# Performance work log

Hardware: AMD Instinct MI355X
Metric: run time of the kernel (lower is better)

Reference implementation:

```python
import jax, jax.numpy as jnp
import numpy as np

N, T, U, V = 8, 200, 50, 500
BLANK = 0
EPS = 1e-10


def setup_inputs() -> dict:
    key = jax.random.key(0)
    k1, k2, k3, k4, k5 = jax.random.split(key, 5)
    logits = jax.random.normal(k1, (N, T, U, V), jnp.float32)
    teacher_logits = jax.random.normal(k2, (N, T, U, V), jnp.float32)
    y = jax.random.randint(k3, (N, U), 1, V)            # padded labels (blank=0 used as pad)
    x_lens = jax.random.randint(k4, (N,), T // 2, T + 1)  # valid encoder frames
    y_lens = jax.random.randint(k5, (N,), U // 2, U + 1)  # valid label lengths
    return {"logits": logits, "teacher_logits": teacher_logits, "y": y,
            "x_lens": x_lens, "y_lens": y_lens}


def reference(logits, teacher_logits, y, x_lens, y_lens):
    # Efficient RNNT-KD: collapse V-dim softmax into 3 classes (label, blank, rest).
    n, t, u, v = logits.shape
    s = jax.nn.softmax(logits, axis=-1)             # (N,T,U,V)
    te = jax.nn.softmax(teacher_logits, axis=-1)    # (N,T,U,V)

    idx = jnp.broadcast_to(y[:, None, :, None], (n, t, u, 1))  # label index per (n,t,u)
    py = jnp.take_along_axis(s, idx, axis=-1)       # (N,T,U,1)
    t_py = jnp.take_along_axis(te, idx, axis=-1)
    blank = s[..., BLANK:BLANK + 1]
    t_blank = te[..., BLANK:BLANK + 1]

    rem = 1.0 - py - blank
    t_rem = 1.0 - t_py - t_blank
    t_rem = jnp.where(t_rem < 0, EPS, t_rem)        # floor negative remainders (in-place set in torch)

    student = jnp.log(jnp.clip(jnp.concatenate([py, blank, rem], axis=-1), EPS, 1.0))  # (N,T,U,3)
    teacher = jnp.concatenate([t_py, t_blank, t_rem], axis=-1)                          # (N,T,U,3)

    t_mask = (jnp.arange(t)[None, :] < x_lens[:, None]).astype(student.dtype)[:, :, None, None]
    u_mask = (jnp.arange(u)[None, :] < y_lens[:, None]).astype(student.dtype)[:, None, :, None]
    m = t_mask * u_mask
    return jnp.stack([student * m, teacher * m])    # (2,N,T,U,3)
```

## Files before the change

kernel.cpp:

```cpp
#include <hip/hip_runtime.h>

#define N_ 8
#define T_ 200
#define U_ 50
#define V_ 500
#define NTU (N_ * T_ * U_)
#define EPSF 1e-10f

__global__ __launch_bounds__(256) void tkd_kernel(
    const float* __restrict__ lg,
    const float* __restrict__ tl,
    const int* __restrict__ y,
    const int* __restrict__ xlen,
    const int* __restrict__ ylen,
    float* __restrict__ out)
{
    const int tid = threadIdx.x;
    const int l   = tid & 15;
    const int row = blockIdx.x * 16 + (tid >> 4);

    const int n  = row / (T_ * U_);
    const int r2 = row - n * (T_ * U_);
    const int t  = r2 / U_;
    const int u  = r2 - t * U_;

    const size_t base = (size_t)row * V_;
    const float4* pa = reinterpret_cast<const float4*>(lg + base);
    const float4* pb = reinterpret_cast<const float4*>(tl + base);

    const int yv = y[n * U_ + u];

    const int ltail = (l <= 12) ? l : 12;
    float4 A[8], B[8];
#pragma unroll
    for (int j = 0; j < 7; ++j) A[j] = pa[j * 16 + l];
    A[7] = pa[112 + ltail];
#pragma unroll
    for (int j = 0; j < 7; ++j) B[j] = pb[j * 16 + l];
    B[7] = pb[112 + ltail];

    __builtin_amdgcn_sched_barrier(0);

    const float ay = lg[base + yv];
    const float by = tl[base + yv];
    const float a0 = lg[base];
    const float b0 = tl[base];

    const float wmask = (l <= 12) ? 1.0f : 0.0f;
    float sA = 0.f, sB = 0.f;
#pragma unroll
    for (int j = 0; j < 7; ++j) {
        sA += __expf(A[j].x); sA += __expf(A[j].y);
        sA += __expf(A[j].z); sA += __expf(A[j].w);
        sB += __expf(B[j].x); sB += __expf(B[j].y);
        sB += __expf(B[j].z); sB += __expf(B[j].w);
    }
    sA += wmask * (__expf(A[7].x) + __expf(A[7].y) + __expf(A[7].z) + __expf(A[7].w));
    sB += wmask * (__expf(B[7].x) + __expf(B[7].y) + __expf(B[7].z) + __expf(B[7].w));

#pragma unroll
    for (int off = 1; off < 16; off <<= 1) {
        sA += __shfl_xor(sA, off, 64);
        sB += __shfl_xor(sB, off, 64);
    }

    if (l == 0) {
        const float invA = 1.0f / sA;
        const float invB = 1.0f / sB;
        const float py   = __expf(ay) * invA;
        const float pbl  = __expf(a0) * invA;
        const float prem = 1.0f - py - pbl;
        const float tpy  = __expf(by) * invB;
        const float tbl  = __expf(b0) * invB;
        float trem = 1.0f - tpy - tbl;
        if (trem < 0.0f) trem = EPSF;

        const float s0 = __logf(fminf(fmaxf(py,   EPSF), 1.0f));
        const float s1 = __logf(fminf(fmaxf(pbl,  EPSF), 1.0f));
        const float s2 = __logf(fminf(fmaxf(prem, EPSF), 1.0f));

        const float mm = ((t < xlen[n]) && (u < ylen[n])) ? 1.0f : 0.0f;

        const size_t o = (size_t)row * 3;
        out[o + 0] = s0 * mm;
        out[o + 1] = s1 * mm;
        out[o + 2] = s2 * mm;
        const size_t o2 = (size_t)NTU * 3 + o;
        out[o2 + 0] = tpy  * mm;
        out[o2 + 1] = tbl  * mm;
        out[o2 + 2] = trem * mm;
    }
}

extern "C" void kernel_launch(void* const* d_in, const int* in_sizes, int n_in,
                              void* d_out, int out_size, void* d_ws, size_t ws_size,
                              hipStream_t stream) {
    const float* lg = (const float*)d_in[0];
    const float* tl = (const float*)d_in[1];
    const int* y    = (const int*)d_in[2];
    const int* xlen = (const int*)d_in[3];
    const int* ylen = (const int*)d_in[4];
    float* out = (float*)d_out;

    tkd_kernel<<<NTU / 16, 256, 0, stream>>>(lg, tl, y, xlen, ylen, out);
}
```

Before: 323.2 us.

## Stage logits tiles into LDS via direct global-to-LDS loads with split waits

Replaces per-thread float4 register loads with buffer loads that write straight into shared memory (global_load_lds). Each block stages 16 rows of both student and teacher logits, 64 KB of LDS in total. A partial vmcnt wait lets the student softmax sum start while teacher data is still arriving. The aim is to cut VGPR pressure and overlap the two streams, but the large LDS footprint limits blocks per CU, and the barriers add synchronisation cost.

Measured after the change: 324.4 us. No clear change (+0.4%).

```diff
diff --git a/kernel.cpp b/kernel.cpp
--- a/kernel.cpp
+++ b/kernel.cpp
@@ -7,6 +7,10 @@
 #define NTU (N_ * T_ * U_)
 #define EPSF 1e-10f
 
+#define ROWS 16
+#define ROWF (ROWS * V_)
+#define FULLC 31
+
 __global__ __launch_bounds__(256) void tkd_kernel(
     const float* __restrict__ lg,
     const float* __restrict__ tl,
@@ -15,54 +19,96 @@
     const int* __restrict__ ylen,
     float* __restrict__ out)
 {
-    const int tid = threadIdx.x;
+    __shared__ float bufA[ROWF];
+    __shared__ float bufB[ROWF];
+
+    const int tid  = threadIdx.x;
+    const int wv   = tid >> 6;
+    const int ln   = tid & 63;
+    const int row0 = blockIdx.x * ROWS;
+
+    const float* gA = lg + (size_t)row0 * V_;
+    const float* gB = tl + (size_t)row0 * V_;
+
+#pragma unroll
+    for (int c = wv; c < FULLC; c += 4) {
+        __builtin_amdgcn_global_load_lds(
+            (const __attribute__((address_space(1))) void*)(gA + c * 256 + ln * 4),
+            (__attribute__((address_space(3))) void*)(&bufA[c * 256 + ln * 4]),
+            16, 0, 0);
+    }
+    if (wv == 3) {
+        __builtin_amdgcn_global_load_lds(
+            (const __attribute__((address_space(1))) void*)(gA + 7936 + ln),
+            (__attribute__((address_space(3))) void*)(&bufA[7936 + ln]),
+            4, 0, 0);
+    }
+#pragma unroll
+    for (int c = wv; c < FULLC; c += 4) {
+        __builtin_amdgcn_global_load_lds(
+            (const __attribute__((address_space(1))) void*)(gB + c * 256 + ln * 4),
+            (__attribute__((address_space(3))) void*)(&bufB[c * 256 + ln * 4]),
+            16, 0, 0);
+    }
+    if (wv == 3) {
+        __builtin_amdgcn_global_load_lds(
+            (const __attribute__((address_space(1))) void*)(gB + 7936 + ln),
+            (__attribute__((address_space(3))) void*)(&bufB[7936 + ln]),
+            4, 0, 0);
+    }
+
+    const int g   = tid >> 4;
     const int l   = tid & 15;
-    const int row = blockIdx.x * 16 + (tid >> 4);
+    const int row = row0 + g;
+    const int n   = row / (T_ * U_);
+    const int r2  = row - n * (T_ * U_);
+    const int t   = r2 / U_;
+    const int u   = r2 - t * U_;
+    const int yv  = y[n * U_ + u];
+    const int xl  = xlen[n];
+    const int yl  = ylen[n];
 
-    const int n  = row / (T_ * U_);
-    const int r2 = row - n * (T_ * U_);
-    const int t  = r2 / U_;
-    const int u  = r2 - t * U_;
+    asm volatile("s_waitcnt vmcnt(8)" ::: "memory");
+    __builtin_amdgcn_s_barrier();
+    asm volatile("" ::: "memory");
 
-    const size_t base = (size_t)row * V_;
-    const float4* pa = reinterpret_cast<const float4*>(lg + base);
-    const float4* pb = reinterpret_cast<const float4*>(tl + base);
-
-    const int yv = y[n * U_ + u];
-
-    const int ltail = (l <= 12) ? l : 12;
-    float4 A[8], B[8];
-#pragma unroll
-    for (int j = 0; j < 7; ++j) A[j] = pa[j * 16 + l];
-    A[7] = pa[112 + ltail];
-#pragma unroll
-    for (int j = 0; j < 7; ++j) B[j] = pb[j * 16 + l];
-    B[7] = pb[112 + ltail];
-
-    __builtin_amdgcn_sched_barrier(0);
-
-    const float ay = lg[base + yv];
-    const float by = tl[base + yv];
-    const float a0 = lg[base];
-    const float b0 = tl[base];
-
+    const float* ra = &bufA[g * V_];
+    const int   ltail = (l <= 12) ? l : 12;
     const float wmask = (l <= 12) ? 1.0f : 0.0f;
-    float sA = 0.f, sB = 0.f;
+    float sA = 0.f;
 #pragma unroll
     for (int j = 0; j < 7; ++j) {
-        sA += __expf(A[j].x); sA += __expf(A[j].y);
-        sA += __expf(A[j].z); sA += __expf(A[j].w);
-        sB += __expf(B[j].x); sB += __expf(B[j].y);
-        sB += __expf(B[j].z); sB += __expf(B[j].w);
+        const float4 v = *reinterpret_cast<const float4*>(ra + (j * 16 + l) * 4);
+        sA += __expf(v.x) + __expf(v.y) + __expf(v.z) + __expf(v.w);
     }
-    sA += wmask * (__expf(A[7].x) + __expf(A[7].y) + __expf(A[7].z) + __expf(A[7].w));
-    sB += wmask * (__expf(B[7].x) + __expf(B[7].y) + __expf(B[7].z) + __expf(B[7].w));
+    {
+        const float4 v = *reinterpret_cast<const float4*>(ra + (112 + ltail) * 4);
+        sA += wmask * (__expf(v.x) + __expf(v.y) + __expf(v.z) + __expf(v.w));
+    }
+#pragma unroll
+    for (int off = 1; off < 16; off <<= 1) sA += __shfl_xor(sA, off, 64);
+    const float ay = ra[yv];
+    const float a0 = ra[0];
 
+    asm volatile("s_waitcnt vmcnt(0)" ::: "memory");
+    __builtin_amdgcn_s_barrier();
+    asm volatile("" ::: "memory");
+
+    const float* rb = &bufB[g * V_];
+    float sB = 0.f;
 #pragma unroll
-    for (int off = 1; off < 16; off <<= 1) {
-        sA += __shfl_xor(sA, off, 64);
-        sB += __shfl_xor(sB, off, 64);
+    for (int j = 0; j < 7; ++j) {
+        const float4 v = *reinterpret_cast<const float4*>(rb + (j * 16 + l) * 4);
+        sB += __expf(v.x) + __expf(v.y) + __expf(v.z) + __expf(v.w);
     }
+    {
+        const float4 v = *reinterpret_cast<const float4*>(rb + (112 + ltail) * 4);
+        sB += wmask * (__expf(v.x) + __expf(v.y) + __expf(v.z) + __expf(v.w));
+    }
+#pragma unroll
+    for (int off = 1; off < 16; off <<= 1) sB += __shfl_xor(sB, off, 64);
+    const float by = rb[yv];
+    const float b0 = rb[0];
 
     if (l == 0) {
         const float invA = 1.0f / sA;
@@ -79,7 +125,7 @@
         const float s1 = __logf(fminf(fmaxf(pbl,  EPSF), 1.0f));
         const float s2 = __logf(fminf(fmaxf(prem, EPSF), 1.0f));
 
-        const float mm = ((t < xlen[n]) && (u < ylen[n])) ? 1.0f : 0.0f;
+        const float mm = ((t < xl) && (u < yl)) ? 1.0f : 0.0f;
 
         const size_t o = (size_t)row * 3;
         out[o + 0] = s0 * mm;
@@ -102,5 +148,5 @@
     const int* ylen = (const int*)d_in[4];
     float* out = (float*)d_out;
 
-    tkd_kernel<<<NTU / 16, 256, 0, stream>>>(lg, tl, y, xlen, ylen, out);
+    tkd_kernel<<<NTU / ROWS, 256, 0, stream>>>(lg, tl, y, xlen, ylen, out);
 }
```

## Assign one full wavefront per row instead of sixteen lanes per row

Applied to the files above, without the earlier changes.

Changes the work split so each 64-lane wavefront handles one (n,t,u) row of 500 logits, with each lane loading two float4 from each tensor instead of eight. The launch uses four rows per block, which means many more blocks and far fewer registers per thread. That should raise memory-level parallelism and occupancy for this bandwidth-bound softmax reduction. In exchange it uses a 6-step cross-lane reduction, removes the explicit sched barrier, and leaves 63 of 64 lanes idle in the scalar epilogue.

After: 319.3 us. Within noise of the previous version (-1.2%).

```diff
diff --git a/kernel.cpp b/kernel.cpp
--- a/kernel.cpp
+++ b/kernel.cpp
@@ -15,56 +15,46 @@
     const int* __restrict__ ylen,
     float* __restrict__ out)
 {
-    const int tid = threadIdx.x;
-    const int l   = tid & 15;
-    const int row = blockIdx.x * 16 + (tid >> 4);
+    const int wid  = (int)((blockIdx.x * 256 + threadIdx.x) >> 6);
+    const int lane = threadIdx.x & 63;
+    if (wid >= NTU) return;
 
-    const int n  = row / (T_ * U_);
-    const int r2 = row - n * (T_ * U_);
+    const int n  = wid / (T_ * U_);
+    const int r2 = wid - n * (T_ * U_);
     const int t  = r2 / U_;
     const int u  = r2 - t * U_;
 
-    const size_t base = (size_t)row * V_;
+    const size_t base = (size_t)wid * V_;
     const float4* pa = reinterpret_cast<const float4*>(lg + base);
     const float4* pb = reinterpret_cast<const float4*>(tl + base);
 
+    const int   l2    = 64 + ((lane <= 60) ? lane : 60);
+    const float wmask = (lane <= 60) ? 1.0f : 0.0f;
+
+    const float4 A1 = pa[lane];
+    const float4 A2 = pa[l2];
+    const float4 B1 = pb[lane];
+    const float4 B2 = pb[l2];
+
     const int yv = y[n * U_ + u];
 
-    const int ltail = (l <= 12) ? l : 12;
-    float4 A[8], B[8];
+    float sA = __expf(A1.x) + __expf(A1.y) + __expf(A1.z) + __expf(A1.w);
+    sA += wmask * (__expf(A2.x) + __expf(A2.y) + __expf(A2.z) + __expf(A2.w));
+    float sB = __expf(B1.x) + __expf(B1.y) + __expf(B1.z) + __expf(B1.w);
+    sB += wmask * (__expf(B2.x) + __expf(B2.y) + __expf(B2.z) + __expf(B2.w));
+
 #pragma unroll
-    for (int j = 0; j < 7; ++j) A[j] = pa[j * 16 + l];
-    A[7] = pa[112 + ltail];
-#pragma unroll
-    for (int j = 0; j < 7; ++j) B[j] = pb[j * 16 + l];
-    B[7] = pb[112 + ltail];
-
-    __builtin_amdgcn_sched_barrier(0);
+    for (int off = 32; off > 0; off >>= 1) {
+        sA += __shfl_xor(sA, off, 64);
+        sB += __shfl_xor(sB, off, 64);
+    }
 
     const float ay = lg[base + yv];
     const float by = tl[base + yv];
     const float a0 = lg[base];
     const float b0 = tl[base];
 
-    const float wmask = (l <= 12) ? 1.0f : 0.0f;
-    float sA = 0.f, sB = 0.f;
-#pragma unroll
-    for (int j = 0; j < 7; ++j) {
-        sA += __expf(A[j].x); sA += __expf(A[j].y);
-        sA += __expf(A[j].z); sA += __expf(A[j].w);
-        sB += __expf(B[j].x); sB += __expf(B[j].y);
-        sB += __expf(B[j].z); sB += __expf(B[j].w);
-    }
-    sA += wmask * (__expf(A[7].x) + __expf(A[7].y) + __expf(A[7].z) + __expf(A[7].w));
-    sB += wmask * (__expf(B[7].x) + __expf(B[7].y) + __expf(B[7].z) + __expf(B[7].w));
-
-#pragma unroll
-    for (int off = 1; off < 16; off <<= 1) {
-        sA += __shfl_xor(sA, off, 64);
-        sB += __shfl_xor(sB, off, 64);
-    }
-
-    if (l == 0) {
+    if (lane == 0) {
         const float invA = 1.0f / sA;
         const float invB = 1.0f / sB;
         const float py   = __expf(ay) * invA;
@@ -81,7 +71,7 @@
 
         const float mm = ((t < xlen[n]) && (u < ylen[n])) ? 1.0f : 0.0f;
 
-        const size_t o = (size_t)row * 3;
+        const size_t o = (size_t)wid * 3;
         out[o + 0] = s0 * mm;
         out[o + 1] = s1 * mm;
         out[o + 2] = s2 * mm;
@@ -102,5 +92,6 @@
     const int* ylen = (const int*)d_in[4];
     float* out = (float*)d_out;
 
-    tkd_kernel<<<NTU / 16, 256, 0, stream>>>(lg, tl, y, xlen, ylen, out);
+    const int blocks = (NTU + 3) / 4;
+    tkd_kernel<<<blocks, 256, 0, stream>>>(lg, tl, y, xlen, ylen, out);
 }
```
